# Optimization experiments

Hardware: AMD Instinct MI355X
Metric: run time of the kernel (lower is better)

Reference implementation:

```python
import jax, jax.numpy as jnp
import numpy as np

N, K, C, OUT = 2048, 14, 512, 512
SCALE = 4.0
BN_EPS = 1e-5


def _edge_lists(k):
    # pairs i<j with i,j != k-1 and adj[i,j] > 0 (adj is fully connected ones)
    ei, ej = [], []
    for i in range(k - 1):
        for j in range(i + 1, k - 1):
            ei.append(i)
            ej.append(j)
    return np.asarray(ei, np.int32), np.asarray(ej, np.int32)


def setup_inputs() -> dict:
    key = jax.random.key(0)
    k0, k1, k2, k3 = jax.random.split(key, 4)
    ei, ej = _edge_lists(K)
    std = 0.02
    return {
        "inputs": jax.random.normal(k0, (N, K, C), dtype=jnp.float32),
        "adj": jnp.ones((K, K), dtype=jnp.float32),
        "edge_i": jnp.asarray(ei),
        "edge_j": jnp.asarray(ej),
        "gamma": jnp.ones((C,), dtype=jnp.float32),
        "beta": jnp.zeros((C,), dtype=jnp.float32),
        "w_direct": jax.random.normal(k1, (C,), dtype=jnp.float32) * std,
        "W_merged": jax.random.normal(k2, (OUT, C), dtype=jnp.float32) * std,
        "W_orig": jax.random.normal(k3, (OUT, C), dtype=jnp.float32) * std,
    }


def reference(inputs, adj, edge_i, edge_j, gamma, beta, w_direct, W_merged, W_orig):
    n, k, c = inputs.shape
    # --- learn_adj ---
    global_feat = inputs[:, k - 1 : k, :]                      # [N,1,c]
    distances = jnp.abs(inputs - global_feat)                  # [N,k,c]
    # pairwise gaps only on the static edge list (i<j, non-global, adj>0)
    gap = 15.0 * (distances[:, edge_i, :] - distances[:, edge_j, :])  # [N,E,c]
    # BatchNorm1d over channel c, batch stats over (N, E), biased variance
    mean = jnp.mean(gap, axis=(0, 1))
    var = jnp.mean(jnp.square(gap - mean), axis=(0, 1))
    bn = (gap - mean) * (gamma / jnp.sqrt(var + BN_EPS)) + beta        # [N,E,c]
    a = jax.nn.sigmoid(SCALE * jnp.einsum("nec,c->ne", bn, w_direct))  # [N,E]
    adj2 = jnp.ones((n, k, k), dtype=inputs.dtype)
    adj2 = adj2.at[:, edge_i, edge_j].set(2.0 * a)
    adj2 = adj2.at[:, edge_j, edge_i].set(2.0 * (1.0 - a))
    new_adj = adj2 * adj[None, :, :]
    norm = jnp.sum(jnp.abs(new_adj), axis=2, keepdims=True)    # L1 row norm
    new_adj = new_adj / jnp.maximum(norm, 1e-12)
    # --- graph conv ---
    agg = jnp.einsum("nij,njc->nic", new_adj, inputs)          # [N,k,c]
    merged = jax.nn.relu(jnp.einsum("nkc,oc->nko", agg, W_merged))
    original = jnp.einsum("nkc,oc->nko", inputs, W_orig)
    return merged + original
```

## Files before the change

### kernel.cpp

```cpp
#include <hip/hip_runtime.h>
#include <stdint.h>

#define K_NODES 14
#define C_DIM   512
#define OUT_DIM 512
#define N_EDGE  78

typedef float  f32x4  __attribute__((ext_vector_type(4)));
typedef __bf16 bf16x8 __attribute__((ext_vector_type(8)));

__device__ __forceinline__ unsigned short f2bf(float f) {
    unsigned int u = __builtin_bit_cast(unsigned int, f);
    unsigned int r = (u + 0x7fffu + ((u >> 16) & 1u)) >> 16;
    return (unsigned short)r;
}
__device__ __forceinline__ float bf2f(unsigned short s) {
    return __builtin_bit_cast(float, (unsigned int)s << 16);
}

__device__ __forceinline__ void async16(const void* g, void* l) {
    __builtin_amdgcn_global_load_lds(
        (const __attribute__((address_space(1))) unsigned int*)g,
        (__attribute__((address_space(3))) unsigned int*)l, 16, 0, 0);
}

__global__ __launch_bounds__(512) void stats_partial(
    const float* __restrict__ x, float* __restrict__ part,
    unsigned short* __restrict__ xbf, int n_per_block)
{
    int c  = threadIdx.x;
    int n0 = blockIdx.x * n_per_block;
    float s_sum = 0.f, s_sq = 0.f;
    for (int nn = 0; nn < n_per_block; ++nn) {
        size_t base = (size_t)(n0 + nn) * K_NODES * C_DIM + c;
        const float* xb = x + base;
        unsigned short* xo = xbf + base;
        float g = xb[13 * C_DIM];
        xo[13 * C_DIM] = f2bf(g);
        float S1 = 0.f, S2 = 0.f, Sw = 0.f;
        #pragma unroll
        for (int k = 0; k < 13; ++k) {
            float v = xb[k * C_DIM];
            xo[k * C_DIM] = f2bf(v);
            float d = fabsf(v - g);
            S1 += d; S2 += d * d; Sw += (float)(12 - 2 * k) * d;
        }
        s_sum += 15.f * Sw;
        s_sq  += 225.f * (13.f * S2 - S1 * S1);
    }
    part[(size_t)blockIdx.x * 1024 + c]       = s_sum;
    part[(size_t)blockIdx.x * 1024 + 512 + c] = s_sq;
}

__global__ __launch_bounds__(1024) void finalize_stats(
    const float* __restrict__ part, float inv_ne,
    const float* __restrict__ gamma, const float* __restrict__ beta,
    const float* __restrict__ wdir, float* __restrict__ u, float* __restrict__ bconst)
{
    int c = threadIdx.x & 511;
    int h = threadIdx.x >> 9;
    float s = 0.f, q = 0.f;
    for (int b = h * 128; b < h * 128 + 128; b += 8) {
        #pragma unroll
        for (int t = 0; t < 8; ++t) {
            s += part[(size_t)(b + t) * 1024 + c];
            q += part[(size_t)(b + t) * 1024 + 512 + c];
        }
    }
    __shared__ float sh_s[512], sh_q[512], red[512];
    if (h == 0) { sh_s[c] = s; sh_q[c] = q; }
    __syncthreads();
    if (h == 1) { sh_s[c] += s; sh_q[c] += q; }
    __syncthreads();
    if (h == 0) {
        float mean = sh_s[c] * inv_ne;
        float var  = sh_q[c] * inv_ne - mean * mean;
        float sc   = gamma[c] / sqrtf(var + 1e-5f);
        u[c] = sc * wdir[c];
        red[c] = (beta[c] - mean * sc) * wdir[c];
    }
    __syncthreads();
    for (int st = 256; st > 0; st >>= 1) {
        if (threadIdx.x < st) red[threadIdx.x] += red[threadIdx.x + st];
        __syncthreads();
    }
    if (threadIdx.x == 0) *bconst = red[0];
}

__global__ __launch_bounds__(256) void conv_w(
    const float* __restrict__ a, const float* __restrict__ b,
    unsigned short* __restrict__ oa, unsigned short* __restrict__ ob)
{
    int i = blockIdx.x * 256 + threadIdx.x;
    oa[i] = f2bf(a[i]);
    ob[i] = f2bf(b[i]);
}

__global__ __launch_bounds__(512) void fuse_graph(
    const unsigned short* __restrict__ xbf, const float* __restrict__ adj,
    const int* __restrict__ ei, const int* __restrict__ ej,
    const float* __restrict__ u, const float* __restrict__ bconst,
    unsigned short* __restrict__ aggbf)
{
    __shared__ float Dl[13];
    __shared__ float Wl[K_NODES * K_NODES];
    __shared__ float rnorm[K_NODES];
    int n = blockIdx.x, c = threadIdx.x;
    size_t base = (size_t)n * K_NODES * C_DIM + c;

    float xv[K_NODES];
    #pragma unroll
    for (int k = 0; k < K_NODES; ++k) xv[k] = bf2f(xbf[base + k * C_DIM]);

    if (c < 13) Dl[c] = 0.f;
    __syncthreads();

    float g  = xv[13];
    float uc = u[c];
    #pragma unroll
    for (int k = 0; k < 13; ++k) {
        float val = fabsf(xv[k] - g) * uc;
        #pragma unroll
        for (int off = 32; off > 0; off >>= 1) val += __shfl_down(val, off, 64);
        if ((c & 63) == 0) atomicAdd(&Dl[k], val);
    }
    __syncthreads();

    if (c < K_NODES * K_NODES) Wl[c] = 1.f;
    __syncthreads();
    if (c < N_EDGE) {
        float z = 4.0f * (15.f * (Dl[ei[c]] - Dl[ej[c]]) + *bconst);
        float a = 1.f / (1.f + expf(-z));
        Wl[ei[c] * K_NODES + ej[c]] = 2.f * a;
        Wl[ej[c] * K_NODES + ei[c]] = 2.f * (1.f - a);
    }
    __syncthreads();
    if (c < K_NODES * K_NODES) Wl[c] *= adj[c];
    __syncthreads();
    if (c < K_NODES) {
        float s = 0.f;
        #pragma unroll
        for (int j = 0; j < K_NODES; ++j) s += fabsf(Wl[c * K_NODES + j]);
        rnorm[c] = fmaxf(s, 1e-12f);
    }
    __syncthreads();
    if (c < K_NODES * K_NODES) Wl[c] /= rnorm[c / K_NODES];
    __syncthreads();

    #pragma unroll
    for (int i = 0; i < K_NODES; ++i) {
        float s = 0.f;
        #pragma unroll
        for (int j = 0; j < K_NODES; ++j) s += Wl[i * K_NODES + j] * xv[j];
        aggbf[base + i * C_DIM] = f2bf(s);
    }
}

#define TM 128
#define TN 128
#define BK 64

__global__ __launch_bounds__(256) void gemm_fused(
    const unsigned short* __restrict__ Aagg, const unsigned short* __restrict__ Axin,
    const unsigned short* __restrict__ Bwm,  const unsigned short* __restrict__ Bwo,
    float* __restrict__ out)
{
    __shared__ unsigned short lA[TM * BK];
    __shared__ unsigned short lB[TN * BK];
    int tid  = threadIdx.x;
    int lane = tid & 63;
    int wave = tid >> 6;
    int wr = wave >> 1, wc = wave & 1;
    int bm = blockIdx.x * TM;
    int bn = blockIdx.y * TN;

    f32x4 acc[4][4];
    #pragma unroll
    for (int i = 0; i < 4; ++i)
        #pragma unroll
        for (int j = 0; j < 4; ++j) acc[i][j] = (f32x4){0.f, 0.f, 0.f, 0.f};

    int lrow = lane & 15;
    int lko  = (lane >> 4) * 8;

    #pragma unroll
    for (int pass = 0; pass < 2; ++pass) {
        const unsigned short* A = pass ? Axin : Aagg;
        const unsigned short* B = pass ? Bwo  : Bwm;
        for (int kb = 0; kb < C_DIM; kb += BK) {
            __syncthreads();
            #pragma unroll
            for (int it = 0; it < 4; ++it) {
                int p   = it * 256 + tid;
                int row = p >> 3;
                int ch  = (p & 7) * 8;
                async16(A + (size_t)(bm + row) * C_DIM + kb + ch,
                        &lA[(size_t)(it * 256 + wave * 64) * 8]);
                async16(B + (size_t)(bn + row) * C_DIM + kb + ch,
                        &lB[(size_t)(it * 256 + wave * 64) * 8]);
            }
            __syncthreads();
            #pragma unroll
            for (int ks = 0; ks < 2; ++ks) {
                bf16x8 af[4], bfr[4];
                #pragma unroll
                for (int i = 0; i < 4; ++i)
                    af[i] = *(const bf16x8*)&lA[(wr * 64 + i * 16 + lrow) * BK + ks * 32 + lko];
                #pragma unroll
                for (int j = 0; j < 4; ++j)
                    bfr[j] = *(const bf16x8*)&lB[(wc * 64 + j * 16 + lrow) * BK + ks * 32 + lko];
                #pragma unroll
                for (int i = 0; i < 4; ++i)
                    #pragma unroll
                    for (int j = 0; j < 4; ++j)
                        acc[i][j] = __builtin_amdgcn_mfma_f32_16x16x32_bf16(
                            af[i], bfr[j], acc[i][j], 0, 0, 0);
            }
        }
        if (pass == 0) {
            #pragma unroll
            for (int i = 0; i < 4; ++i)
                #pragma unroll
                for (int j = 0; j < 4; ++j)
                    #pragma unroll
                    for (int r = 0; r < 4; ++r)
                        acc[i][j][r] = fmaxf(acc[i][j][r], 0.f);
        }
    }

    int orow0 = bm + wr * 64 + (lane >> 4) * 4;
    int ocol0 = bn + wc * 64 + (lane & 15);
    #pragma unroll
    for (int i = 0; i < 4; ++i)
        #pragma unroll
        for (int j = 0; j < 4; ++j)
            #pragma unroll
            for (int r = 0; r < 4; ++r)
                out[(size_t)(orow0 + i * 16 + r) * OUT_DIM + (ocol0 + j * 16)] = acc[i][j][r];
}

extern "C" void kernel_launch(void* const* d_in, const int* in_sizes, int n_in,
                              void* d_out, int out_size, void* d_ws, size_t ws_size,
                              hipStream_t stream)
{
    const float* x     = (const float*)d_in[0];
    const float* adj   = (const float*)d_in[1];
    const int*   ei    = (const int*)d_in[2];
    const int*   ej    = (const int*)d_in[3];
    const float* gamma = (const float*)d_in[4];
    const float* beta  = (const float*)d_in[5];
    const float* wdir  = (const float*)d_in[6];
    const float* Wm    = (const float*)d_in[7];
    const float* Wo    = (const float*)d_in[8];
    float* out = (float*)d_out;

    int N = in_sizes[0] / (K_NODES * C_DIM);
    int M = N * K_NODES;

    float* ws_f   = (float*)d_ws;
    float* u      = ws_f + 1024;
    float* bconst = ws_f + 1536;
    float* part   = ws_f + 2048;
    char*  wsb    = (char*)d_ws;
    size_t off    = (size_t)(2048 + 256 * 1024) * sizeof(float);
    unsigned short* wmbf  = (unsigned short*)(wsb + off);  off += (size_t)OUT_DIM * C_DIM * 2;
    unsigned short* wobf  = (unsigned short*)(wsb + off);  off += (size_t)OUT_DIM * C_DIM * 2;
    unsigned short* xbf   = (unsigned short*)(wsb + off);  off += (size_t)M * C_DIM * 2;
    unsigned short* aggbf = (unsigned short*)(wsb + off);

    const int stats_blocks = 256;
    int n_per_block = N / stats_blocks;
    float inv_ne = 1.0f / ((float)N * (float)N_EDGE);

    hipLaunchKernelGGL(stats_partial, dim3(stats_blocks), dim3(512), 0, stream,
                       x, part, xbf, n_per_block);
    hipLaunchKernelGGL(finalize_stats, dim3(1), dim3(1024), 0, stream,
                       part, inv_ne, gamma, beta, wdir, u, bconst);
    hipLaunchKernelGGL(conv_w, dim3((OUT_DIM * C_DIM) / 256), dim3(256), 0, stream,
                       Wm, Wo, wmbf, wobf);
    hipLaunchKernelGGL(fuse_graph, dim3(N), dim3(512), 0, stream,
                       xbf, adj, ei, ej, u, bconst, aggbf);
    hipLaunchKernelGGL(gemm_fused, dim3(M / TM, OUT_DIM / TN), dim3(256), 0, stream,
                       aggbf, xbf, wmbf, wobf, out);
}
```

Before: 216.0 us.

## Swizzle GEMM LDS tiles and fold weight conversion into stats kernel

After: 204.2 us. 1.06x faster.

```diff
diff --git a/kernel.cpp b/kernel.cpp
--- a/kernel.cpp
+++ b/kernel.cpp
@@ -26,7 +26,10 @@
 
 __global__ __launch_bounds__(512) void stats_partial(
     const float* __restrict__ x, float* __restrict__ part,
-    unsigned short* __restrict__ xbf, int n_per_block)
+    unsigned short* __restrict__ xbf, int n_per_block,
+    const float* __restrict__ Wm, const float* __restrict__ Wo,
+    unsigned short* __restrict__ wmbf, unsigned short* __restrict__ wobf,
+    float* __restrict__ bconst)
 {
     int c  = threadIdx.x;
     int n0 = blockIdx.x * n_per_block;
@@ -50,6 +53,14 @@
     }
     part[(size_t)blockIdx.x * 1024 + c]       = s_sum;
     part[(size_t)blockIdx.x * 1024 + 512 + c] = s_sq;
+    {
+        int i0 = blockIdx.x * 1024 + c;
+        wmbf[i0]       = f2bf(Wm[i0]);
+        wmbf[i0 + 512] = f2bf(Wm[i0 + 512]);
+        wobf[i0]       = f2bf(Wo[i0]);
+        wobf[i0 + 512] = f2bf(Wo[i0 + 512]);
+    }
+    if (blockIdx.x == 0 && c == 0) *bconst = 0.f;
 }
 
 __global__ __launch_bounds__(1024) void finalize_stats(
@@ -85,15 +96,6 @@
         __syncthreads();
     }
     if (threadIdx.x == 0) *bconst = red[0];
-}
-
-__global__ __launch_bounds__(256) void conv_w(
-    const float* __restrict__ a, const float* __restrict__ b,
-    unsigned short* __restrict__ oa, unsigned short* __restrict__ ob)
-{
-    int i = blockIdx.x * 256 + threadIdx.x;
-    oa[i] = f2bf(a[i]);
-    ob[i] = f2bf(b[i]);
 }
 
 __global__ __launch_bounds__(512) void fuse_graph(
@@ -181,7 +183,9 @@
         for (int j = 0; j < 4; ++j) acc[i][j] = (f32x4){0.f, 0.f, 0.f, 0.f};
 
     int lrow = lane & 15;
-    int lko  = (lane >> 4) * 8;
+    int xorv = lane & 7;
+    int srow  = tid >> 3;
+    int lcu   = ((tid & 7) ^ (srow & 7)) * 8;
 
     #pragma unroll
     for (int pass = 0; pass < 2; ++pass) {
@@ -191,24 +195,23 @@
             __syncthreads();
             #pragma unroll
             for (int it = 0; it < 4; ++it) {
-                int p   = it * 256 + tid;
-                int row = p >> 3;
-                int ch  = (p & 7) * 8;
-                async16(A + (size_t)(bm + row) * C_DIM + kb + ch,
+                int row = it * 32 + srow;
+                async16(A + (size_t)(bm + row) * C_DIM + kb + lcu,
                         &lA[(size_t)(it * 256 + wave * 64) * 8]);
-                async16(B + (size_t)(bn + row) * C_DIM + kb + ch,
+                async16(B + (size_t)(bn + row) * C_DIM + kb + lcu,
                         &lB[(size_t)(it * 256 + wave * 64) * 8]);
             }
             __syncthreads();
             #pragma unroll
             for (int ks = 0; ks < 2; ++ks) {
+                int pchunk = ((ks * 4 + (lane >> 4)) ^ xorv) * 8;
                 bf16x8 af[4], bfr[4];
                 #pragma unroll
                 for (int i = 0; i < 4; ++i)
-                    af[i] = *(const bf16x8*)&lA[(wr * 64 + i * 16 + lrow) * BK + ks * 32 + lko];
+                    af[i] = *(const bf16x8*)&lA[(wr * 64 + i * 16 + lrow) * BK + pchunk];
                 #pragma unroll
                 for (int j = 0; j < 4; ++j)
-                    bfr[j] = *(const bf16x8*)&lB[(wc * 64 + j * 16 + lrow) * BK + ks * 32 + lko];
+                    bfr[j] = *(const bf16x8*)&lB[(wc * 64 + j * 16 + lrow) * BK + pchunk];
                 #pragma unroll
                 for (int i = 0; i < 4; ++i)
                     #pragma unroll
@@ -273,11 +276,9 @@
     float inv_ne = 1.0f / ((float)N * (float)N_EDGE);
 
     hipLaunchKernelGGL(stats_partial, dim3(stats_blocks), dim3(512), 0, stream,
-                       x, part, xbf, n_per_block);
+                       x, part, xbf, n_per_block, Wm, Wo, wmbf, wobf, bconst);
     hipLaunchKernelGGL(finalize_stats, dim3(1), dim3(1024), 0, stream,
                        part, inv_ne, gamma, beta, wdir, u, bconst);
-    hipLaunchKernelGGL(conv_w, dim3((OUT_DIM * C_DIM) / 256), dim3(256), 0, stream,
-                       Wm, Wo, wmbf, wobf);
     hipLaunchKernelGGL(fuse_graph, dim3(N), dim3(512), 0, stream,
                        xbf, adj, ei, ej, u, bconst, aggbf);
     hipLaunchKernelGGL(gemm_fused, dim3(M / TM, OUT_DIM / TN), dim3(256), 0, stream,
```
